# Kernel optimization log

Measured on AMD Instinct MI355X. Metric: run time of the kernel, lower is better.

## Reference

```python
import jax, jax.numpy as jnp
import numpy as np

NUM_CLASSES = 1000
FEAT_DIM = 512
BATCH = 65536


def setup_inputs() -> dict:
    key = jax.random.key(0)
    k1, k2, k3 = jax.random.split(key, 3)
    features = jax.random.normal(k1, (BATCH, FEAT_DIM), dtype=jnp.float32)
    centers = jax.random.normal(k2, (NUM_CLASSES, FEAT_DIM), dtype=jnp.float32)
    labels = jax.random.randint(k3, (BATCH,), 0, NUM_CLASSES, dtype=jnp.int64)
    return {"features": features, "centers": centers, "labels": labels}


def reference(features, centers, labels):
    # Torch loop: for each class j with count>0, add F.mse_loss(z_j, center_j)
    # = sum_{i: l_i=j} ||f_i - c_j||^2 / (count_j * feat_dim); final /= batch_size.
    batch_size, feat_dim = features.shape
    num_classes = centers.shape[0]
    labels = labels.astype(jnp.int32)
    c = jax.lax.stop_gradient(centers)  # centers are detached in the original
    # per-sample squared distance to its own class center: [batch]
    diff = features - c[labels]
    d = jnp.sum(diff * diff, axis=-1)
    # per-class sums and counts in one segment-reduce pass
    sums = jax.ops.segment_sum(d, labels, num_segments=num_classes)
    counts = jax.ops.segment_sum(jnp.ones_like(d), labels, num_segments=num_classes)
    per_class = jnp.where(counts > 0, sums / (counts * feat_dim), 0.0)
    return jnp.sum(per_class) / batch_size
```

## Files before the change

### kernel.cpp

```cpp
#include <hip/hip_runtime.h>


#define WAVE 64
#define HPAD 1024

__global__ __launch_bounds__(256) void center_dist_kernel(
    const float* __restrict__ features,
    const float* __restrict__ centers,
    const int*   __restrict__ labels,
    float* __restrict__ dvals,
    int batch, int feat)
{
    const int wave_in_block = threadIdx.x >> 6;
    const int lane          = threadIdx.x & 63;
    const int sample        = blockIdx.x * 4 + wave_in_block;
    if (sample >= batch) return;

    const int label = labels[sample];

    const float4* __restrict__ f4 =
        (const float4*)(features + (size_t)sample * feat);
    const float4* __restrict__ c4 =
        (const float4*)(centers + (size_t)label * feat);

    float acc = 0.0f;
    const int n4 = feat >> 2;
#pragma unroll 2
    for (int idx = lane; idx < n4; idx += WAVE) {
        float4 fv = f4[idx];
        float4 cv = c4[idx];
        float dx = fv.x - cv.x;
        float dy = fv.y - cv.y;
        float dz = fv.z - cv.z;
        float dw = fv.w - cv.w;
        acc += dx * dx + dy * dy;
        acc += dz * dz + dw * dw;
    }

#pragma unroll
    for (int off = 32; off > 0; off >>= 1)
        acc += __shfl_down(acc, off, WAVE);

    if (lane == 0) dvals[sample] = acc;
}

__global__ __launch_bounds__(256) void hist_kernel(
    const int* __restrict__ labels,
    unsigned int* __restrict__ hist,
    int batch, int nclass)
{
    __shared__ unsigned int h[HPAD];
    for (int j = threadIdx.x; j < HPAD; j += 256) h[j] = 0u;
    __syncthreads();

    const int base = blockIdx.x * 1024;
    for (int k = threadIdx.x; k < 1024; k += 256) {
        const int i = base + k;
        if (i < batch) atomicAdd(&h[labels[i]], 1u);
    }
    __syncthreads();

    unsigned int* __restrict__ out = hist + (size_t)blockIdx.x * HPAD;
    for (int j = threadIdx.x; j < nclass; j += 256) out[j] = h[j];
}

__global__ __launch_bounds__(1024) void counts_kernel(
    const unsigned int* __restrict__ hist,
    float* __restrict__ invcnt,
    int nclass, int feat, int nblocks)
{
    for (int j = threadIdx.x; j < nclass; j += 1024) {
        unsigned int n = 0;
#pragma unroll 4
        for (int b = 0; b < nblocks; ++b)
            n += hist[(size_t)b * HPAD + j];
        invcnt[j] = (n > 0u) ? 1.0f / ((float)n * (float)feat) : 0.0f;
    }
}

__global__ __launch_bounds__(1024) void final_kernel(
    const float* __restrict__ dvals,
    const int*   __restrict__ labels,
    const float* __restrict__ invcnt,
    float* __restrict__ out,
    int batch)
{
    float acc = 0.0f;
    for (int i = threadIdx.x; i < batch; i += 1024)
        acc += dvals[i] * invcnt[labels[i]];

#pragma unroll
    for (int off = 32; off > 0; off >>= 1)
        acc += __shfl_down(acc, off, WAVE);

    __shared__ float warp_part[16];
    const int lane = threadIdx.x & 63;
    const int wid  = threadIdx.x >> 6;
    if (lane == 0) warp_part[wid] = acc;
    __syncthreads();

    if (threadIdx.x < WAVE) {
        float v = (threadIdx.x < 16) ? warp_part[threadIdx.x] : 0.0f;
#pragma unroll
        for (int off = 8; off > 0; off >>= 1)
            v += __shfl_down(v, off, WAVE);
        if (threadIdx.x == 0) out[0] = v / (float)batch;
    }
}

extern "C" void kernel_launch(void* const* d_in, const int* in_sizes, int n_in,
                              void* d_out, int out_size, void* d_ws, size_t ws_size,
                              hipStream_t stream) {
    const float* features = (const float*)d_in[0];
    const float* centers  = (const float*)d_in[1];
    const int*   labels   = (const int*)d_in[2];

    const int batch  = in_sizes[2];
    const int feat   = in_sizes[0] / batch;
    const int nclass = in_sizes[1] / feat;

    const int nblocks_h = (batch + 1023) / 1024;

    float*        dvals  = (float*)d_ws;
    unsigned int* hist   = (unsigned int*)(dvals + batch);
    float*        invcnt = (float*)(hist + (size_t)nblocks_h * HPAD);

    center_dist_kernel<<<(batch + 3) / 4, 256, 0, stream>>>(
        features, centers, labels, dvals, batch, feat);

    hist_kernel<<<nblocks_h, 256, 0, stream>>>(labels, hist, batch, nclass);

    counts_kernel<<<1, 1024, 0, stream>>>(hist, invcnt, nclass, feat, nblocks_h);

    final_kernel<<<1, 1024, 0, stream>>>(dvals, labels, invcnt,
                                         (float*)d_out, batch);
}
```

Before: 230.7 us.

## Fuse count lookup into distance kernel via transposed 64-column histogram

Histogram now runs first with 64 blocks writing a transposed class-by-block table. Each distance wave then reads its label's 64 partial counts, one per lane, reduces them alongside the distance, and scales its term directly. Per-block partial sums replace the per-sample dvals array. This removes the serial counts_kernel and the single-block final pass over the whole batch. In exchange the distance kernel now depends on the histogram, and the histogram has only 64 blocks, so its parallelism is lower.

```diff
diff --git a/kernel.cpp b/kernel.cpp
--- a/kernel.cpp
+++ b/kernel.cpp
@@ -2,92 +2,91 @@
 
 
 #define WAVE 64
+#define NCOL 64
 #define HPAD 1024
+
+__global__ __launch_bounds__(256) void hist_kernel(
+    const int* __restrict__ labels,
+    unsigned int* __restrict__ histT,
+    int batch, int nclass, int slab)
+{
+    __shared__ unsigned int h[HPAD];
+    for (int j = threadIdx.x; j < HPAD; j += 256) h[j] = 0u;
+    __syncthreads();
+
+    const int b  = blockIdx.x;
+    const int lo = b * slab;
+    int hi = lo + slab; if (hi > batch) hi = batch;
+    for (int i = lo + threadIdx.x; i < hi; i += 256)
+        atomicAdd(&h[labels[i]], 1u);
+    __syncthreads();
+
+    for (int j = threadIdx.x; j < nclass; j += 256)
+        histT[(size_t)j * NCOL + b] = h[j];
+}
 
 __global__ __launch_bounds__(256) void center_dist_kernel(
     const float* __restrict__ features,
     const float* __restrict__ centers,
     const int*   __restrict__ labels,
-    float* __restrict__ dvals,
+    const unsigned int* __restrict__ histT,
+    float* __restrict__ partials,
     int batch, int feat)
 {
-    const int wave_in_block = threadIdx.x >> 6;
-    const int lane          = threadIdx.x & 63;
-    const int sample        = blockIdx.x * 4 + wave_in_block;
-    if (sample >= batch) return;
+    const int wib    = threadIdx.x >> 6;
+    const int lane   = threadIdx.x & 63;
+    const int sample = blockIdx.x * 4 + wib;
 
-    const int label = labels[sample];
+    __shared__ float wsum[4];
+    float term = 0.0f;
 
-    const float4* __restrict__ f4 =
-        (const float4*)(features + (size_t)sample * feat);
-    const float4* __restrict__ c4 =
-        (const float4*)(centers + (size_t)label * feat);
+    if (sample < batch) {
+        const int label = labels[sample];
 
-    float acc = 0.0f;
-    const int n4 = feat >> 2;
+        unsigned int nl = histT[(size_t)label * NCOL + lane];
+
+        const float4* __restrict__ f4 =
+            (const float4*)(features + (size_t)sample * feat);
+        const float4* __restrict__ c4 =
+            (const float4*)(centers + (size_t)label * feat);
+
+        float acc = 0.0f;
+        const int n4 = feat >> 2;
 #pragma unroll 2
-    for (int idx = lane; idx < n4; idx += WAVE) {
-        float4 fv = f4[idx];
-        float4 cv = c4[idx];
-        float dx = fv.x - cv.x;
-        float dy = fv.y - cv.y;
-        float dz = fv.z - cv.z;
-        float dw = fv.w - cv.w;
-        acc += dx * dx + dy * dy;
-        acc += dz * dz + dw * dw;
+        for (int idx = lane; idx < n4; idx += WAVE) {
+            float4 fv = f4[idx];
+            float4 cv = c4[idx];
+            float dx = fv.x - cv.x;
+            float dy = fv.y - cv.y;
+            float dz = fv.z - cv.z;
+            float dw = fv.w - cv.w;
+            acc += dx * dx + dy * dy;
+            acc += dz * dz + dw * dw;
+        }
+
+        int n = (int)nl;
+#pragma unroll
+        for (int off = 32; off > 0; off >>= 1) {
+            acc += __shfl_down(acc, off, WAVE);
+            n   += __shfl_down(n,   off, WAVE);
+        }
+        term = acc / ((float)n * (float)feat);
     }
 
-#pragma unroll
-    for (int off = 32; off > 0; off >>= 1)
-        acc += __shfl_down(acc, off, WAVE);
-
-    if (lane == 0) dvals[sample] = acc;
+    if (lane == 0) wsum[wib] = term;
+    __syncthreads();
+    if (threadIdx.x == 0)
+        partials[blockIdx.x] = wsum[0] + wsum[1] + wsum[2] + wsum[3];
 }
 
-__global__ __launch_bounds__(256) void hist_kernel(
-    const int* __restrict__ labels,
-    unsigned int* __restrict__ hist,
-    int batch, int nclass)
-{
-    __shared__ unsigned int h[HPAD];
-    for (int j = threadIdx.x; j < HPAD; j += 256) h[j] = 0u;
-    __syncthreads();
-
-    const int base = blockIdx.x * 1024;
-    for (int k = threadIdx.x; k < 1024; k += 256) {
-        const int i = base + k;
-        if (i < batch) atomicAdd(&h[labels[i]], 1u);
-    }
-    __syncthreads();
-
-    unsigned int* __restrict__ out = hist + (size_t)blockIdx.x * HPAD;
-    for (int j = threadIdx.x; j < nclass; j += 256) out[j] = h[j];
-}
-
-__global__ __launch_bounds__(1024) void counts_kernel(
-    const unsigned int* __restrict__ hist,
-    float* __restrict__ invcnt,
-    int nclass, int feat, int nblocks)
-{
-    for (int j = threadIdx.x; j < nclass; j += 1024) {
-        unsigned int n = 0;
-#pragma unroll 4
-        for (int b = 0; b < nblocks; ++b)
-            n += hist[(size_t)b * HPAD + j];
-        invcnt[j] = (n > 0u) ? 1.0f / ((float)n * (float)feat) : 0.0f;
-    }
-}
-
-__global__ __launch_bounds__(1024) void final_kernel(
-    const float* __restrict__ dvals,
-    const int*   __restrict__ labels,
-    const float* __restrict__ invcnt,
-    float* __restrict__ out,
-    int batch)
+__global__ __launch_bounds__(1024) void reduce_kernel(
+    const float* __restrict__ partials, float* __restrict__ out,
+    int n, int batch)
 {
     float acc = 0.0f;
-    for (int i = threadIdx.x; i < batch; i += 1024)
-        acc += dvals[i] * invcnt[labels[i]];
+#pragma unroll 4
+    for (int i = threadIdx.x; i < n; i += 1024)
+        acc += partials[i];
 
 #pragma unroll
     for (int off = 32; off > 0; off >>= 1)
@@ -119,19 +118,17 @@
     const int feat   = in_sizes[0] / batch;
     const int nclass = in_sizes[1] / feat;
 
-    const int nblocks_h = (batch + 1023) / 1024;
+    const int slab        = (batch + NCOL - 1) / NCOL;
+    const int dist_blocks = (batch + 3) / 4;
 
-    float*        dvals  = (float*)d_ws;
-    unsigned int* hist   = (unsigned int*)(dvals + batch);
-    float*        invcnt = (float*)(hist + (size_t)nblocks_h * HPAD);
+    unsigned int* histT    = (unsigned int*)d_ws;
+    float*        partials = (float*)(histT + (size_t)HPAD * NCOL);
 
-    center_dist_kernel<<<(batch + 3) / 4, 256, 0, stream>>>(
-        features, centers, labels, dvals, batch, feat);
+    hist_kernel<<<NCOL, 256, 0, stream>>>(labels, histT, batch, nclass, slab);
 
-    hist_kernel<<<nblocks_h, 256, 0, stream>>>(labels, hist, batch, nclass);
+    center_dist_kernel<<<dist_blocks, 256, 0, stream>>>(
+        features, centers, labels, histT, partials, batch, feat);
 
-    counts_kernel<<<1, 1024, 0, stream>>>(hist, invcnt, nclass, feat, nblocks_h);
-
-    final_kernel<<<1, 1024, 0, stream>>>(dvals, labels, invcnt,
-                                         (float*)d_out, batch);
+    reduce_kernel<<<1, 1024, 0, stream>>>(partials, (float*)d_out,
+                                          dist_blocks, batch);
 }
```

Measured after the change: 195.1 us. -15.5%, faster.
